# Kernel tuning notes

Measured on AMD Instinct MI355X. Metric: run time of the kernel, lower is better.

## Reference

```python
import jax, jax.numpy as jnp
import numpy as np

B_, N_, H_ = 4, 256, 32          # batch, nodes, neighbors (edges = B*N*H)
NC_IN, NC_OUT = 16, 16
NUM_FREQ, D_OUT, M_IN = 3, 3, 3  # degree_in = degree_out = 1 -> 2*1+1
EDGE_DIM, HID = 16, 64
LN_EPS = 1e-5


def _ln(x, gamma):
    # torch F.layer_norm over last dim, beta fixed at zero
    mu = jnp.mean(x, axis=-1, keepdims=True)
    var = jnp.var(x, axis=-1, keepdims=True)
    return (x - mu) * jax.lax.rsqrt(var + LN_EPS) * gamma


def setup_inputs() -> dict:
    key = jax.random.key(0)
    ks = jax.random.split(key, 8)

    def lin(k, fin, fout):
        lim = 1.0 / np.sqrt(fin)
        kw, kb = jax.random.split(k)
        W = jax.random.uniform(kw, (fin, fout), jnp.float32, -lim, lim)
        b = jax.random.uniform(kb, (fout,), jnp.float32, -lim, lim)
        return W, b

    W1, b1 = lin(ks[0], EDGE_DIM + 1, HID)
    W2, b2 = lin(ks[1], HID, HID)
    W3, b3 = lin(ks[2], HID, NUM_FREQ * NC_IN * NC_OUT)
    return {
        "feat": jax.random.normal(ks[3], (B_, N_, H_, EDGE_DIM + 1), jnp.float32),
        "basis": jax.random.normal(ks[4], (B_, N_, H_, D_OUT, M_IN, NUM_FREQ), jnp.float32),
        "W1": W1, "b1": b1, "g1": jnp.ones((HID,), jnp.float32),
        "W2": W2, "b2": b2, "g2": jnp.ones((HID,), jnp.float32),
        "W3": W3, "b3": b3,
    }


def reference(feat, basis, W1, b1, g1, W2, b2, g2, W3, b3):
    # radial MLP: Linear -> SiLU -> LN -> Linear -> SiLU -> LN -> Linear
    h = _ln(jax.nn.silu(feat @ W1 + b1), g1)
    h = _ln(jax.nn.silu(h @ W2 + b2), g2)
    r = h @ W3 + b3                                   # (b, n, k, o*i*f)
    R = r.reshape(*r.shape[:-1], NC_OUT, NC_IN, NUM_FREQ)  # '(o i f) -> o i f'
    # per-frequency multiply-accumulate: sum_f R[...,o,i,f] * B[...,d,m,f]
    out = jnp.einsum('bnkoif,bnkdmf->bnkodim', R, basis)   # (b,n,k,o,d,i,m)
    b, n, k = out.shape[:3]
    # contiguous reshape matches torch rearrange + view: (b,n,k, d_out*nc_out, nc_in*m_in)
    return out.reshape(b, n, k, NC_OUT * D_OUT, NC_IN * M_IN)
```

## Files before the change

kernel.cpp:

```cpp
#include <hip/hip_runtime.h>

#define E_TOTAL 32768
#define F_IN 17
#define HID 64
#define NJ 768

using bf16x8 = __attribute__((ext_vector_type(8))) short;
using f32x4  = __attribute__((ext_vector_type(4))) float;

__device__ __forceinline__ unsigned short f2bf(float x){
    unsigned u = __float_as_uint(x);
    u += 0x7fffu + ((u >> 16) & 1u);
    return (unsigned short)(u >> 16);
}

__global__ __launch_bounds__(256) void prep_w3(const float* __restrict__ W3,
                                               unsigned short* __restrict__ w3t){
    int t = blockIdx.x * 256 + threadIdx.x;
    int n = t >> 6, k = t & 63;
    w3t[t] = f2bf(W3[k * NJ + n]);
}

__global__ __launch_bounds__(256) void mlp_kernel(const float* __restrict__ feat,
        const float* __restrict__ W1, const float* __restrict__ b1, const float* __restrict__ g1,
        const float* __restrict__ W2, const float* __restrict__ b2, const float* __restrict__ g2,
        unsigned short* __restrict__ hb){
    __shared__ float sW1[F_IN * HID];
    __shared__ float sW2[HID * HID];
    __shared__ float sC[4 * HID];
    __shared__ float sFeat[16 * F_IN];
    __shared__ __align__(16) float sH1[16][HID];

    int tid = threadIdx.x;
    int e0  = blockIdx.x * 16;
    for (int i = tid; i < F_IN * HID; i += 256) sW1[i] = W1[i];
    for (int i = tid; i < HID * HID; i += 256) sW2[i] = W2[i];
    if (tid < 64) { sC[tid] = b1[tid]; sC[64 + tid] = g1[tid];
                    sC[128 + tid] = b2[tid]; sC[192 + tid] = g2[tid]; }
    for (int i = tid; i < 16 * F_IN; i += 256) sFeat[i] = feat[(size_t)e0 * F_IN + i];
    __syncthreads();

    int j = tid & 63, wv = tid >> 6;
    float acc[4], x[4], s1[4], s2[4];

    #pragma unroll
    for (int q = 0; q < 4; ++q) acc[q] = sC[j];
    for (int k = 0; k < F_IN; ++k){
        float w = sW1[k * 64 + j];
        #pragma unroll
        for (int q = 0; q < 4; ++q) acc[q] += sFeat[(wv * 4 + q) * F_IN + k] * w;
    }
    #pragma unroll
    for (int q = 0; q < 4; ++q){
        float a = acc[q];
        float sg = 1.0f / (1.0f + __expf(-a));
        x[q] = a * sg; s1[q] = x[q]; s2[q] = x[q] * x[q];
    }
    #pragma unroll
    for (int m = 1; m < 64; m <<= 1){
        #pragma unroll
        for (int q = 0; q < 4; ++q){
            s1[q] += __shfl_xor(s1[q], m);
            s2[q] += __shfl_xor(s2[q], m);
        }
    }
    #pragma unroll
    for (int q = 0; q < 4; ++q){
        float mu  = s1[q] * (1.0f / 64.0f);
        float var = s2[q] * (1.0f / 64.0f) - mu * mu;
        float rs  = rsqrtf(var + 1e-5f);
        sH1[wv * 4 + q][j] = (x[q] - mu) * rs * sC[64 + j];
    }

    #pragma unroll
    for (int q = 0; q < 4; ++q) acc[q] = sC[128 + j];
    for (int k4 = 0; k4 < 16; ++k4){
        float hv[4][4];
        #pragma unroll
        for (int q = 0; q < 4; ++q) *(float4*)hv[q] = *(const float4*)&sH1[wv * 4 + q][k4 * 4];
        #pragma unroll
        for (int kk = 0; kk < 4; ++kk){
            float w = sW2[(k4 * 4 + kk) * 64 + j];
            #pragma unroll
            for (int q = 0; q < 4; ++q) acc[q] += hv[q][kk] * w;
        }
    }
    #pragma unroll
    for (int q = 0; q < 4; ++q){
        float a = acc[q];
        float sg = 1.0f / (1.0f + __expf(-a));
        x[q] = a * sg; s1[q] = x[q]; s2[q] = x[q] * x[q];
    }
    #pragma unroll
    for (int m = 1; m < 64; m <<= 1){
        #pragma unroll
        for (int q = 0; q < 4; ++q){
            s1[q] += __shfl_xor(s1[q], m);
            s2[q] += __shfl_xor(s2[q], m);
        }
    }
    #pragma unroll
    for (int q = 0; q < 4; ++q){
        float mu  = s1[q] * (1.0f / 64.0f);
        float var = s2[q] * (1.0f / 64.0f) - mu * mu;
        float rs  = rsqrtf(var + 1e-5f);
        float h2  = (x[q] - mu) * rs * sC[192 + j];
        hb[(size_t)(e0 + wv * 4 + q) * 64 + j] = f2bf(h2);
    }
}

__global__ __launch_bounds__(256, 3) void tp_kernel(const unsigned short* __restrict__ hb,
        const unsigned short* __restrict__ w3t, const float* __restrict__ b3,
        const float* __restrict__ basis, float* __restrict__ out){
    __shared__ __align__(16) float sR[16 * 196];
    __shared__ __align__(16) float sO[16 * 580];

    int tid = threadIdx.x;
    int e0  = blockIdx.x * 16;

    int wv = tid >> 6, l = tid & 63;
    int col = l & 15, kg = l >> 4;

    const unsigned short* hrow = hb + (size_t)(e0 + col) * 64;
    bf16x8 a0 = *(const bf16x8*)(hrow + kg * 8);
    bf16x8 a1 = *(const bf16x8*)(hrow + 32 + kg * 8);

    int e_loc = wv * 4 + kg;
    int s     = col;
    float bs[27];
    const float* bp = basis + (size_t)(e0 + e_loc) * 27;
    #pragma unroll
    for (int z = 0; z < 27; ++z) bs[z] = bp[z];

    float* outB = out + (size_t)e0 * 2304;
    const float* Rrow = sR + e_loc * 196;
    float* Orow = sO + e_loc * 580;

    for (int c4 = 0; c4 < 4; ++c4){
        if (c4 > 0){
            #pragma unroll
            for (int k = 0; k < 9; ++k){
                int idx4 = k * 256 + tid;
                int e = idx4 / 144, c = idx4 - e * 144;
                f32x4 v = *(const f32x4*)(sO + e * 580 + c * 4);
                *(f32x4*)(outB + (size_t)e * 2304 + (c4 - 1) * 576 + c * 4) = v;
            }
        }
        #pragma unroll
        for (int t = 0; t < 3; ++t){
            int n0 = c4 * 192 + wv * 48 + t * 16;
            const unsigned short* wrow = w3t + (size_t)(n0 + col) * 64;
            bf16x8 bb0 = *(const bf16x8*)(wrow + kg * 8);
            bf16x8 bb1 = *(const bf16x8*)(wrow + 32 + kg * 8);
            f32x4 acc = {0.f, 0.f, 0.f, 0.f};
            acc = __builtin_amdgcn_mfma_f32_16x16x32_bf16(a0, bb0, acc, 0, 0, 0);
            acc = __builtin_amdgcn_mfma_f32_16x16x32_bf16(a1, bb1, acc, 0, 0, 0);
            float bj = b3[n0 + col];
            int cL = wv * 48 + t * 16 + col;
            #pragma unroll
            for (int r = 0; r < 4; ++r)
                sR[(kg * 4 + r) * 196 + cL] = acc[r] + bj;
        }
        __syncthreads();

        #pragma unroll
        for (int t2 = 0; t2 < 4; ++t2){
            const float* rp = Rrow + t2 * 48 + s * 3;
            float r0 = rp[0], r1 = rp[1], r2 = rp[2];
            #pragma unroll
            for (int d = 0; d < 3; ++d){
                float* p = Orow + t2 * 144 + d * 48 + s * 3;
                int z = d * 9;
                p[0] = r0 * bs[z + 0] + r1 * bs[z + 1] + r2 * bs[z + 2];
                p[1] = r0 * bs[z + 3] + r1 * bs[z + 4] + r2 * bs[z + 5];
                p[2] = r0 * bs[z + 6] + r1 * bs[z + 7] + r2 * bs[z + 8];
            }
        }
        __syncthreads();
    }

    #pragma unroll
    for (int k = 0; k < 9; ++k){
        int idx4 = k * 256 + tid;
        int e = idx4 / 144, c = idx4 - e * 144;
        f32x4 v = *(const f32x4*)(sO + e * 580 + c * 4);
        *(f32x4*)(outB + (size_t)e * 2304 + 3 * 576 + c * 4) = v;
    }
}

extern "C" void kernel_launch(void* const* d_in, const int* in_sizes, int n_in,
                              void* d_out, int out_size, void* d_ws, size_t ws_size,
                              hipStream_t stream) {
    const float* feat  = (const float*)d_in[0];
    const float* basis = (const float*)d_in[1];
    const float* W1 = (const float*)d_in[2];
    const float* b1 = (const float*)d_in[3];
    const float* g1 = (const float*)d_in[4];
    const float* W2 = (const float*)d_in[5];
    const float* b2 = (const float*)d_in[6];
    const float* g2 = (const float*)d_in[7];
    const float* W3 = (const float*)d_in[8];
    const float* b3 = (const float*)d_in[9];
    float* out = (float*)d_out;

    unsigned short* hbuf = (unsigned short*)d_ws;
    unsigned short* w3t  = hbuf + (size_t)E_TOTAL * HID;

    prep_w3<<<NJ * HID / 256, 256, 0, stream>>>(W3, w3t);
    mlp_kernel<<<E_TOTAL / 16, 256, 0, stream>>>(feat, W1, b1, g1, W2, b2, g2, hbuf);
    tp_kernel<<<E_TOTAL / 16, 256, 0, stream>>>(hbuf, w3t, b3, basis, out);
}
```

Before: 360.0 us.

## Fuse radial MLP into tensor-product kernel and use DPP wave reductions

```diff
diff --git a/kernel.cpp b/kernel.cpp
--- a/kernel.cpp
+++ b/kernel.cpp
@@ -12,6 +12,16 @@
     unsigned u = __float_as_uint(x);
     u += 0x7fffu + ((u >> 16) & 1u);
     return (unsigned short)(u >> 16);
+}
+
+__device__ __forceinline__ float wave_sum(float x){
+    x += __int_as_float(__builtin_amdgcn_update_dpp(0, __float_as_int(x), 0x111, 0xf, 0xf, true));
+    x += __int_as_float(__builtin_amdgcn_update_dpp(0, __float_as_int(x), 0x112, 0xf, 0xf, true));
+    x += __int_as_float(__builtin_amdgcn_update_dpp(0, __float_as_int(x), 0x114, 0xf, 0xf, true));
+    x += __int_as_float(__builtin_amdgcn_update_dpp(0, __float_as_int(x), 0x118, 0xf, 0xf, true));
+    x += __int_as_float(__builtin_amdgcn_update_dpp(0, __float_as_int(x), 0x142, 0xa, 0xf, true));
+    x += __int_as_float(__builtin_amdgcn_update_dpp(0, __float_as_int(x), 0x143, 0xc, 0xf, true));
+    return __int_as_float(__builtin_amdgcn_readlane(__float_as_int(x), 63));
 }
 
 __global__ __launch_bounds__(256) void prep_w3(const float* __restrict__ W3,
@@ -21,55 +31,61 @@
     w3t[t] = f2bf(W3[k * NJ + n]);
 }
 
-__global__ __launch_bounds__(256) void mlp_kernel(const float* __restrict__ feat,
+__global__ __launch_bounds__(256, 3) void fused_kernel(const float* __restrict__ feat,
         const float* __restrict__ W1, const float* __restrict__ b1, const float* __restrict__ g1,
         const float* __restrict__ W2, const float* __restrict__ b2, const float* __restrict__ g2,
-        unsigned short* __restrict__ hb){
-    __shared__ float sW1[F_IN * HID];
-    __shared__ float sW2[HID * HID];
-    __shared__ float sC[4 * HID];
-    __shared__ float sFeat[16 * F_IN];
-    __shared__ __align__(16) float sH1[16][HID];
+        const unsigned short* __restrict__ w3t, const float* __restrict__ b3,
+        const float* __restrict__ basis, float* __restrict__ out){
+    __shared__ __align__(16) char smem[51968];
+    unsigned short* sH  = (unsigned short*)smem;
+    char* rgn = smem + 2304;
+    float* sW1 = (float*)rgn;
+    float* sW2 = (float*)(rgn + 4352);
+    float* sC  = (float*)(rgn + 20736);
+    float* sFe = (float*)(rgn + 21760);
+    float* sH1 = (float*)(rgn + 22848);
+    float* sR  = (float*)rgn;
+    float* sO  = (float*)(rgn + 12544);
 
     int tid = threadIdx.x;
     int e0  = blockIdx.x * 16;
-    for (int i = tid; i < F_IN * HID; i += 256) sW1[i] = W1[i];
-    for (int i = tid; i < HID * HID; i += 256) sW2[i] = W2[i];
-    if (tid < 64) { sC[tid] = b1[tid]; sC[64 + tid] = g1[tid];
-                    sC[128 + tid] = b2[tid]; sC[192 + tid] = g2[tid]; }
-    for (int i = tid; i < 16 * F_IN; i += 256) sFeat[i] = feat[(size_t)e0 * F_IN + i];
+    int wv = tid >> 6, l = tid & 63;
+    int j = l;
+    int col = l & 15, kg = l >> 4;
+    int e_loc = wv * 4 + kg;
+    int s = col;
+
+    for (int i = tid; i < 272; i += 256) ((f32x4*)sW1)[i] = ((const f32x4*)W1)[i];
+    #pragma unroll
+    for (int k = 0; k < 4; ++k) ((f32x4*)sW2)[k * 256 + tid] = ((const f32x4*)W2)[k * 256 + tid];
+    if (tid < 64){
+        int g = tid >> 4, r = tid & 15;
+        const float* src = (g == 0) ? b1 : (g == 1) ? g1 : (g == 2) ? b2 : g2;
+        ((f32x4*)sC)[tid] = ((const f32x4*)src)[r];
+    }
+    if (tid < 68) ((f32x4*)sFe)[tid] = ((const f32x4*)(feat + (size_t)e0 * F_IN))[tid];
     __syncthreads();
 
-    int j = tid & 63, wv = tid >> 6;
-    float acc[4], x[4], s1[4], s2[4];
+    float acc[4], x[4];
 
     #pragma unroll
     for (int q = 0; q < 4; ++q) acc[q] = sC[j];
     for (int k = 0; k < F_IN; ++k){
         float w = sW1[k * 64 + j];
         #pragma unroll
-        for (int q = 0; q < 4; ++q) acc[q] += sFeat[(wv * 4 + q) * F_IN + k] * w;
+        for (int q = 0; q < 4; ++q) acc[q] += sFe[(wv * 4 + q) * F_IN + k] * w;
     }
     #pragma unroll
     for (int q = 0; q < 4; ++q){
         float a = acc[q];
         float sg = 1.0f / (1.0f + __expf(-a));
-        x[q] = a * sg; s1[q] = x[q]; s2[q] = x[q] * x[q];
-    }
-    #pragma unroll
-    for (int m = 1; m < 64; m <<= 1){
-        #pragma unroll
-        for (int q = 0; q < 4; ++q){
-            s1[q] += __shfl_xor(s1[q], m);
-            s2[q] += __shfl_xor(s2[q], m);
-        }
-    }
-    #pragma unroll
-    for (int q = 0; q < 4; ++q){
-        float mu  = s1[q] * (1.0f / 64.0f);
-        float var = s2[q] * (1.0f / 64.0f) - mu * mu;
+        x[q] = a * sg;
+        float s1 = wave_sum(x[q]);
+        float s2 = wave_sum(x[q] * x[q]);
+        float mu  = s1 * (1.0f / 64.0f);
+        float var = s2 * (1.0f / 64.0f) - mu * mu;
         float rs  = rsqrtf(var + 1e-5f);
-        sH1[wv * 4 + q][j] = (x[q] - mu) * rs * sC[64 + j];
+        sH1[(wv * 4 + q) * 64 + j] = (x[q] - mu) * rs * sC[64 + j];
     }
 
     #pragma unroll
@@ -77,7 +93,7 @@
     for (int k4 = 0; k4 < 16; ++k4){
         float hv[4][4];
         #pragma unroll
-        for (int q = 0; q < 4; ++q) *(float4*)hv[q] = *(const float4*)&sH1[wv * 4 + q][k4 * 4];
+        for (int q = 0; q < 4; ++q) *(float4*)hv[q] = *(const float4*)&sH1[(wv * 4 + q) * 64 + k4 * 4];
         #pragma unroll
         for (int kk = 0; kk < 4; ++kk){
             float w = sW2[(k4 * 4 + kk) * 64 + j];
@@ -89,48 +105,25 @@
     for (int q = 0; q < 4; ++q){
         float a = acc[q];
         float sg = 1.0f / (1.0f + __expf(-a));
-        x[q] = a * sg; s1[q] = x[q]; s2[q] = x[q] * x[q];
-    }
-    #pragma unroll
-    for (int m = 1; m < 64; m <<= 1){
-        #pragma unroll
-        for (int q = 0; q < 4; ++q){
-            s1[q] += __shfl_xor(s1[q], m);
-            s2[q] += __shfl_xor(s2[q], m);
-        }
-    }
-    #pragma unroll
-    for (int q = 0; q < 4; ++q){
-        float mu  = s1[q] * (1.0f / 64.0f);
-        float var = s2[q] * (1.0f / 64.0f) - mu * mu;
+        x[q] = a * sg;
+        float s1 = wave_sum(x[q]);
+        float s2 = wave_sum(x[q] * x[q]);
+        float mu  = s1 * (1.0f / 64.0f);
+        float var = s2 * (1.0f / 64.0f) - mu * mu;
         float rs  = rsqrtf(var + 1e-5f);
-        float h2  = (x[q] - mu) * rs * sC[192 + j];
-        hb[(size_t)(e0 + wv * 4 + q) * 64 + j] = f2bf(h2);
-    }
-}
-
-__global__ __launch_bounds__(256, 3) void tp_kernel(const unsigned short* __restrict__ hb,
-        const unsigned short* __restrict__ w3t, const float* __restrict__ b3,
-        const float* __restrict__ basis, float* __restrict__ out){
-    __shared__ __align__(16) float sR[16 * 196];
-    __shared__ __align__(16) float sO[16 * 580];
-
-    int tid = threadIdx.x;
-    int e0  = blockIdx.x * 16;
-
-    int wv = tid >> 6, l = tid & 63;
-    int col = l & 15, kg = l >> 4;
-
-    const unsigned short* hrow = hb + (size_t)(e0 + col) * 64;
-    bf16x8 a0 = *(const bf16x8*)(hrow + kg * 8);
-    bf16x8 a1 = *(const bf16x8*)(hrow + 32 + kg * 8);
-
-    int e_loc = wv * 4 + kg;
-    int s     = col;
+        sH[(wv * 4 + q) * 72 + j] = f2bf((x[q] - mu) * rs * sC[192 + j]);
+    }
+
     float bs[27];
-    const float* bp = basis + (size_t)(e0 + e_loc) * 27;
-    #pragma unroll
-    for (int z = 0; z < 27; ++z) bs[z] = bp[z];
+    {
+        const float* bp = basis + (size_t)(e0 + e_loc) * 27;
+        #pragma unroll
+        for (int z = 0; z < 27; ++z) bs[z] = bp[z];
+    }
+    __syncthreads();
+
+    bf16x8 a0 = *(const bf16x8*)(sH + col * 72 + kg * 8);
+    bf16x8 a1 = *(const bf16x8*)(sH + col * 72 + 32 + kg * 8);
 
     float* outB = out + (size_t)e0 * 2304;
     const float* Rrow = sR + e_loc * 196;
@@ -152,14 +145,14 @@
             const unsigned short* wrow = w3t + (size_t)(n0 + col) * 64;
             bf16x8 bb0 = *(const bf16x8*)(wrow + kg * 8);
             bf16x8 bb1 = *(const bf16x8*)(wrow + 32 + kg * 8);
-            f32x4 acc = {0.f, 0.f, 0.f, 0.f};
-            acc = __builtin_amdgcn_mfma_f32_16x16x32_bf16(a0, bb0, acc, 0, 0, 0);
-            acc = __builtin_amdgcn_mfma_f32_16x16x32_bf16(a1, bb1, acc, 0, 0, 0);
+            f32x4 acc2 = {0.f, 0.f, 0.f, 0.f};
+            acc2 = __builtin_amdgcn_mfma_f32_16x16x32_bf16(a0, bb0, acc2, 0, 0, 0);
+            acc2 = __builtin_amdgcn_mfma_f32_16x16x32_bf16(a1, bb1, acc2, 0, 0, 0);
             float bj = b3[n0 + col];
             int cL = wv * 48 + t * 16 + col;
             #pragma unroll
             for (int r = 0; r < 4; ++r)
-                sR[(kg * 4 + r) * 196 + cL] = acc[r] + bj;
+                sR[(kg * 4 + r) * 196 + cL] = acc2[r] + bj;
         }
         __syncthreads();
 
@@ -203,10 +196,9 @@
     const float* b3 = (const float*)d_in[9];
     float* out = (float*)d_out;
 
-    unsigned short* hbuf = (unsigned short*)d_ws;
-    unsigned short* w3t  = hbuf + (size_t)E_TOTAL * HID;
+    unsigned short* w3t = (unsigned short*)d_ws;
 
     prep_w3<<<NJ * HID / 256, 256, 0, stream>>>(W3, w3t);
-    mlp_kernel<<<E_TOTAL / 16, 256, 0, stream>>>(feat, W1, b1, g1, W2, b2, g2, hbuf);
-    tp_kernel<<<E_TOTAL / 16, 256, 0, stream>>>(hbuf, w3t, b3, basis, out);
-}
+    fused_kernel<<<E_TOTAL / 16, 256, 0, stream>>>(feat, W1, b1, g1, W2, b2, g2,
+                                                   w3t, b3, basis, out);
+}
```

After: 348.9 us. -3.1%, faster.
